# Performance work log

Measured on AMD Instinct MI355X. Metric: run time of the kernel, lower is better.

Reference implementation:

```python
import jax, jax.numpy as jnp
import numpy as np

D_MODEL, D_STATE, D_CONV, EXPAND, N_HEADS = 768, 64, 4, 2, 12
D_INNER = D_MODEL * EXPAND           # 1536
HEAD_DIM = D_INNER // N_HEADS        # 128
IN_PROJ = D_INNER * 2 + N_HEADS * D_STATE * 2 + N_HEADS  # 4620
EPS = 1e-5


def setup_inputs() -> dict:
    key = jax.random.key(0)
    ks = jax.random.split(key, 8)
    s = lambda fan_in: 1.0 / np.sqrt(fan_in)
    return {
        "x": jax.random.normal(ks[0], (1, 1024, D_MODEL), dtype=jnp.float32),
        "W_in": jax.random.normal(ks[1], (IN_PROJ, D_MODEL), dtype=jnp.float32) * s(D_MODEL),
        "conv_w": jax.random.normal(ks[2], (D_INNER, D_CONV), dtype=jnp.float32) * s(D_CONV),
        "conv_b": jnp.zeros((D_INNER,), dtype=jnp.float32),
        "A_log": jnp.full((N_HEADS,), np.log(0.5), dtype=jnp.float32),
        "Dp": jnp.ones((N_HEADS,), dtype=jnp.float32),
        "dt_bias": jnp.zeros((N_HEADS,), dtype=jnp.float32),
        "W_out": jax.random.normal(ks[3], (D_MODEL, D_INNER), dtype=jnp.float32) * s(D_INNER),
        "norm_w": jnp.ones((D_INNER,), dtype=jnp.float32),
    }


def _causal_conv1d(x, w, b):
    # x: (B,L,Din), depthwise causal conv with kernel size D_CONV
    L = x.shape[1]
    xp = jnp.pad(x, ((0, 0), (D_CONV - 1, 0), (0, 0)))
    y = b
    for i in range(D_CONV):  # fixed small kernel, unrolled
        y = y + xp[:, i:i + L, :] * w[:, i]
    return y


def reference(x, W_in, conv_w, conv_b, A_log, Dp, dt_bias, W_out, norm_w):
    B_sz, L, _ = x.shape
    nh, ds, hd = N_HEADS, D_STATE, HEAD_DIM
    proj = jnp.einsum('bld,pd->blp', x, W_in)
    z = proj[:, :, :D_INNER]
    x_ssm = proj[:, :, D_INNER:2 * D_INNER]
    o = 2 * D_INNER
    Bm = proj[:, :, o:o + nh * ds].reshape(B_sz, L, nh, ds)
    Cm = proj[:, :, o + nh * ds:o + 2 * nh * ds].reshape(B_sz, L, nh, ds)
    dt_r = proj[:, :, o + 2 * nh * ds:]
    dt = jax.nn.softplus(dt_r) + dt_bias[None, None, :]          # (B,L,nh)

    x_ssm = jax.nn.silu(_causal_conv1d(x_ssm, conv_w, conv_b))
    x_ssm = x_ssm.reshape(B_sz, L, nh, hd)

    A = -jnp.exp(A_log)                                          # (nh,)
    log_decay = A[None, None, :] * dt                            # (B,L,nh)
    Phi = jnp.cumsum(log_decay, axis=1)
    dB = dt[..., None] * Bm                                      # (B,L,nh,ds)
    # b: (B,L,nh,hd,ds) outer product
    b = dB[:, :, :, None, :] * x_ssm[..., None]
    max_exp = 80.0
    exp_neg_Phi = jnp.exp(jnp.minimum(-Phi, max_exp))[..., None, None]
    b_cumsum = jnp.cumsum(exp_neg_Phi * b, axis=1)
    h = jnp.exp(Phi)[..., None, None] * b_cumsum                 # (B,L,nh,hd,ds)
    y = jnp.sum(Cm[:, :, :, None, :] * h, axis=-1)               # (B,L,nh,hd)
    y = y + Dp[None, None, :, None] * x_ssm
    y = y.reshape(B_sz, L, D_INNER)

    # RMSNorm then gate
    rms = jax.lax.rsqrt(jnp.mean(y * y, axis=-1, keepdims=True) + EPS)
    y = y * rms * norm_w
    y = y * jax.nn.silu(z)
    return jnp.einsum('bli,di->bld', y, W_out)
```

## Files before the change

kernel.cpp:

```cpp
#include <hip/hip_runtime.h>
#include <cmath>

#define LSEQ   1024
#define NPROJ  4620
#define NPADW  4736
#define DINNER 1536
#define NH     12
#define HDIM   128
#define OFF_Z  0
#define OFF_X  1536
#define OFF_B  3072
#define OFF_C  3840
#define OFF_DT 4608

typedef unsigned short u16;
typedef unsigned int u32;
typedef short bf16x8 __attribute__((ext_vector_type(8)));
typedef float f32x4 __attribute__((ext_vector_type(4)));

__device__ inline u16 f2b(float f) {
  unsigned u = __float_as_uint(f);
  return (u16)((u + 0x7fffu + ((u >> 16) & 1u)) >> 16);
}
__device__ inline float b2f(u16 h) { return __uint_as_float(((unsigned)h) << 16); }
__device__ inline u32 pk2(float a, float b) { return (u32)f2b(a) | ((u32)f2b(b) << 16); }

__device__ inline void gll16(const void* g, void* l) {
  __builtin_amdgcn_global_load_lds((const __attribute__((address_space(1))) void*)g,
                                   (__attribute__((address_space(3))) void*)l, 16, 0, 0);
}

#define S0N 196608
#define S1N 909312
#define S1V 887040
#define S2N 294912
__global__ __launch_bounds__(256) void ksplit_all(const float* __restrict__ x,
    const float* __restrict__ Wi, const float* __restrict__ Wo,
    u16* __restrict__ Ah, u16* __restrict__ Wh, u16* __restrict__ Woh) {
  int i = blockIdx.x * 256 + threadIdx.x;
  const float* src; u16* hi; int j, valid;
  if (i < S0N)            { src = x;  hi = Ah;  j = i;              valid = S0N; }
  else if (i < S0N + S1N) { src = Wi; hi = Wh;  j = i - S0N;        valid = S1V; }
  else                    { src = Wo; hi = Woh; j = i - S0N - S1N;  valid = S2N; }
  float4 v = (j < valid) ? ((const float4*)src)[j] : make_float4(0.f, 0.f, 0.f, 0.f);
  ((uint2*)hi)[j] = make_uint2(pk2(v.x, v.y), pk2(v.z, v.w));
}

template<int BM, int BN, int MAP, bool NG>
__global__ __launch_bounds__(256) void gemm1(const u16* __restrict__ Ah,
    const u16* __restrict__ Wh, float* __restrict__ C,
    int lda, int ldw, int Ksl, int Nreal, int ldc) {
  constexpr int PLA = BM * 64;
  constexpr int IA = BM / 8, ITOT = IA + BN / 8;
  constexpr int FRn = BN / 32;
  __shared__ u16 lds[PLA + BN * 64];
  const int tid = threadIdx.x;
  const int l = tid & 63, w = tid >> 6;
  const int wm = w >> 1, wn = w & 1;
  const int kg = l >> 4, li = l & 15;

  int b = blockIdx.x, m0, n0, koff;
  float* Cp = C;
  if (MAP == 0) {
    int xcd = b & 7, idx = b >> 3;
    m0 = (idx & 15) * 64;
    n0 = (xcd * 5 + (idx >> 4)) * 128;
    koff = 0;
    if (NG && n0 >= NPADW) return;
  } else {
    int xcd = b & 7, idx = b >> 3;
    int gg = xcd * 6 + (idx >> 4);
    m0 = (idx & 15) * 64;
    n0 = (gg % 12) * 64;
    koff = (gg / 12) * 384;
    Cp = C + (size_t)(gg / 12) * LSEQ * ldc;
  }

  const int srcg = ((l & 7) ^ (l >> 3)) * 8;
  auto stage = [&](int t) {
    const int k0 = koff + t * 64;
    for (int q = w; q < ITOT; q += 4) {
      const u16* gb; int r0b, ldk, dst;
      if (q < IA) { gb = Ah; r0b = m0 + 8 * q;        dst = 8 * q * 64;              ldk = lda; }
      else        { gb = Wh; r0b = n0 + 8 * (q - IA); dst = PLA + 8 * (q - IA) * 64; ldk = ldw; }
      gll16(gb + (size_t)(r0b + (l >> 3)) * ldk + k0 + srcg, &lds[dst]);
    }
  };
  auto rd = [&](int region, int row, int ks) -> bf16x8 {
    return *(const bf16x8*)&lds[region + row * 64 + (((ks * 4 + kg) ^ (row & 7)) << 3)];
  };

  f32x4 acc[2][FRn];
#pragma unroll
  for (int m = 0; m < 2; ++m)
#pragma unroll
    for (int n = 0; n < FRn; ++n) acc[m][n] = (f32x4){0.f, 0.f, 0.f, 0.f};

  const int NT = Ksl / 64;
  stage(0);
  asm volatile("s_waitcnt vmcnt(0)" ::: "memory");
  __syncthreads();
  for (int t = 0; t < NT; ++t) {
    bf16x8 af[2][2], wf[FRn][2];
#pragma unroll
    for (int ks = 0; ks < 2; ++ks) {
#pragma unroll
      for (int m = 0; m < 2; ++m)
        af[m][ks] = rd(0, wm * 32 + m * 16 + li, ks);
#pragma unroll
      for (int n = 0; n < FRn; ++n)
        wf[n][ks] = rd(PLA, wn * (BN / 2) + n * 16 + li, ks);
    }
    __syncthreads();
    if (t + 1 < NT) stage(t + 1);
#pragma unroll
    for (int ks = 0; ks < 2; ++ks)
#pragma unroll
      for (int m = 0; m < 2; ++m)
#pragma unroll
        for (int n = 0; n < FRn; ++n)
          acc[m][n] = __builtin_amdgcn_mfma_f32_16x16x32_bf16(af[m][ks], wf[n][ks], acc[m][n], 0, 0, 0);
    if (t + 1 < NT) {
      asm volatile("s_waitcnt vmcnt(0)" ::: "memory");
      __syncthreads();
    }
  }
#pragma unroll
  for (int m = 0; m < 2; ++m) {
    int rbase = m0 + wm * 32 + m * 16 + kg * 4;
#pragma unroll
    for (int n = 0; n < FRn; ++n) {
      int col = n0 + wn * (BN / 2) + n * 16 + li;
      if (!NG || col < Nreal) {
#pragma unroll
        for (int r = 0; r < 4; ++r)
          Cp[(size_t)(rbase + r) * ldc + col] = acc[m][n][r];
      }
    }
  }
}

__global__ __launch_bounds__(256) void addk(const float* __restrict__ P,
    const float* __restrict__ rmsacc, float* __restrict__ out) {
  const int S = LSEQ * 768 / 4;
  int i = blockIdx.x * 256 + threadIdx.x;
  int t = i / 192;
  float rms = rsqrtf(rmsacc[t] * (1.f / 1536.f) + 1e-5f);
  float4 a = ((const float4*)P)[i];
  float4 b = ((const float4*)P)[i + S];
  float4 c = ((const float4*)P)[i + 2 * S];
  float4 d = ((const float4*)P)[i + 3 * S];
  ((float4*)out)[i] = make_float4((a.x + b.x + c.x + d.x) * rms,
                                  (a.y + b.y + c.y + d.y) * rms,
                                  (a.z + b.z + c.z + d.z) * rms,
                                  (a.w + b.w + c.w + d.w) * rms);
}

__global__ __launch_bounds__(256) void dtphi(const float* __restrict__ proj,
    const float* __restrict__ A_log, const float* __restrict__ dt_bias,
    float* __restrict__ Phi, float* __restrict__ dts, float* __restrict__ rmsacc) {
  int h = blockIdx.x, tid = threadIdx.x;
  if (h < 4) rmsacc[h * 256 + tid] = 0.f;
  float Ac = -expf(A_log[h]);
  float bb = dt_bias[h];
  float v[4], s = 0.f;
#pragma unroll
  for (int u = 0; u < 4; ++u) {
    int t = tid * 4 + u;
    float xr = proj[(size_t)t * NPROJ + OFF_DT + h];
    float sp = (xr > 20.f) ? xr : log1pf(expf(xr));
    v[u] = sp + bb;
    s += v[u];
  }
  int lane = tid & 63, wv = tid >> 6;
  float ps = s;
#pragma unroll
  for (int d = 1; d < 64; d <<= 1) {
    float o = __shfl_up(ps, d);
    if (lane >= d) ps += o;
  }
  __shared__ float wsum[4];
  if (lane == 63) wsum[wv] = ps;
  __syncthreads();
  float off = 0.f;
  for (int w = 0; w < wv; ++w) off += wsum[w];
  float run = off + ps - s;
#pragma unroll
  for (int u = 0; u < 4; ++u) {
    int t = tid * 4 + u;
    run += v[u];
    Phi[t * NH + h] = Ac * run;
    dts[t * NH + h] = v[u];
  }
}

__global__ __launch_bounds__(256) void conv_state(const float* __restrict__ proj,
    const float* __restrict__ cw, const float* __restrict__ cb,
    const float* __restrict__ Phi, const float* __restrict__ dts,
    u16* __restrict__ xactT, float* __restrict__ SlocF) {
  const int k = blockIdx.x, h = blockIdx.y, tid = threadIdx.x;
  const int l = tid & 63, w = tid >> 6, kg = l >> 4, li = l & 15;
  __shared__ u16 Bw[4096];
  __shared__ u16 Xt[8192];
  __shared__ float wS[64];
  const int s0 = k * 64;
  if (tid < 64) {
    float pe = Phi[(s0 + 63) * NH + h];
    float p  = Phi[(s0 + tid) * NH + h];
    wS[tid] = expf(pe + fminf(-p, 80.f)) * dts[(s0 + tid) * NH + h];
  }
  __syncthreads();
#pragma unroll
  for (int u = 0; u < 4; ++u) {
    int idx = tid + u * 256, s = idx >> 4, q = (idx & 15) * 4;
    float4 v = *(const float4*)(proj + (size_t)(s0 + s) * NPROJ + OFF_B + h * 64 + q);
    float ws_ = wS[s];
    float vv[4] = {v.x, v.y, v.z, v.w};
#pragma unroll
    for (int j = 0; j < 4; ++j) {
      int d = q + j;
      Bw[d * 64 + (((s >> 3) ^ (d & 7)) << 3) + (s & 7)] = f2b(vv[j] * ws_);
    }
  }
  {
    int c = tid & 127, th = tid >> 7;
    int cg = h * HDIM + c;
    float w0 = cw[cg * 4], w1 = cw[cg * 4 + 1], w2 = cw[cg * 4 + 2], w3 = cw[cg * 4 + 3];
    float bias = cb[cg];
    int tb = s0 + th * 32;
    auto P = [&](int t) { return (t >= 0) ? proj[(size_t)t * NPROJ + OFF_X + cg] : 0.f; };
    float x0 = P(tb - 3), x1 = P(tb - 2), x2 = P(tb - 1);
    u32 pkb[16];
    float prev = 0.f;
#pragma unroll
    for (int i = 0; i < 32; ++i) {
      float x3 = P(tb + i);
      float a = bias;
      a = fmaf(x0, w0, a); a = fmaf(x1, w1, a); a = fmaf(x2, w2, a); a = fmaf(x3, w3, a);
      float sv = a / (1.f + expf(-a));
      if (i & 1) pkb[i >> 1] = pk2(prev, sv); else prev = sv;
      x0 = x1; x1 = x2; x2 = x3;
    }
#pragma unroll
    for (int g = 0; g < 4; ++g) {
      int sg = th * 4 + g;
      *(uint4*)&Xt[c * 64 + ((sg ^ (c & 7)) << 3)] =
          make_uint4(pkb[g * 4], pkb[g * 4 + 1], pkb[g * 4 + 2], pkb[g * 4 + 3]);
    }
    size_t xo = ((size_t)(k * NH + h) * 128 + c) * 64 + th * 32;
#pragma unroll
    for (int g = 0; g < 4; ++g)
      *(uint4*)(xactT + xo + g * 8) =
          make_uint4(pkb[g * 4], pkb[g * 4 + 1], pkb[g * 4 + 2], pkb[g * 4 + 3]);
  }
  __syncthreads();
  const int wm = w >> 1, wn = w & 1;
  auto rd = [&](const u16* reg, int row, int ks) -> bf16x8 {
    return *(const bf16x8*)&reg[row * 64 + (((ks * 4 + kg) ^ (row & 7)) << 3)];
  };
  f32x4 acc[4][2];
#pragma unroll
  for (int m = 0; m < 4; ++m)
#pragma unroll
    for (int n = 0; n < 2; ++n) acc[m][n] = (f32x4){0.f, 0.f, 0.f, 0.f};
#pragma unroll
  for (int ks = 0; ks < 2; ++ks) {
    bf16x8 xf[4], bf[2];
#pragma unroll
    for (int m = 0; m < 4; ++m) xf[m] = rd(Xt, wm * 64 + m * 16 + li, ks);
#pragma unroll
    for (int n = 0; n < 2; ++n) bf[n] = rd(Bw, wn * 32 + n * 16 + li, ks);
#pragma unroll
    for (int m = 0; m < 4; ++m)
#pragma unroll
      for (int n = 0; n < 2; ++n)
        acc[m][n] = __builtin_amdgcn_mfma_f32_16x16x32_bf16(xf[m], bf[n], acc[m][n], 0, 0, 0);
  }
  float* dst = SlocF + (((size_t)(k * NH + h)) << 13);
#pragma unroll
  for (int m = 0; m < 4; ++m)
#pragma unroll
    for (int n = 0; n < 2; ++n)
#pragma unroll
      for (int r = 0; r < 4; ++r) {
        int c = wm * 64 + m * 16 + kg * 4 + r;
        int d = wn * 32 + n * 16 + li;
        dst[c * 64 + d] = acc[m][n][r];
      }
}

__global__ __launch_bounds__(256) void chunk_scan(const float* __restrict__ SlocF,
    u16* __restrict__ SlocT, const float* __restrict__ Phi) {
  int b = blockIdx.x;
  int h = b >> 5;
  int e = (b & 31) * 256 + threadIdx.x;
  float run = SlocF[((size_t)h << 13) + e];
  SlocT[((size_t)h << 13) + e] = f2b(run);
#pragma unroll
  for (int k = 1; k < 16; ++k) {
    float lam = expf(Phi[(k * 64 + 63) * NH + h] - Phi[(k * 64 - 1) * NH + h]);
    size_t o = ((size_t)(k * NH + h) << 13) + e;
    run = fmaf(lam, run, SlocF[o]);
    SlocT[o] = f2b(run);
  }
}

__global__ __launch_bounds__(256) void ssm_out(const float* __restrict__ proj,
    const u16* __restrict__ xactT, const float* __restrict__ Phi,
    const float* __restrict__ dts, const float* __restrict__ Dp,
    const u16* __restrict__ SlocT, const float* __restrict__ nw,
    u16* __restrict__ Yh, float* __restrict__ rmsacc) {
  const int k = blockIdx.x, h = blockIdx.y, zh = blockIdx.z, tid = threadIdx.x;
  const int l = tid & 63, w = tid >> 6, kg = l >> 4, li = l & 15;
  const int wm = w >> 1, wn = w & 1;
  __shared__ u16 Cs[4096], Bs[4096], Ps[4096], Xs[4096], Ss[4096];
  __shared__ float phiT[64], eSs[64], dSs[64], eTs[64];
  __shared__ float sq[64], nws[64];
  const int t0 = k * 64;
  const int srcg = ((l & 7) ^ (l >> 3)) * 8;
  {
#pragma unroll
    for (int j = 0; j < 2; ++j) {
      int rb = w * 16 + j * 8;
      gll16(xactT + ((size_t)(k * NH + h) * 128 + zh * 64 + rb + (l >> 3)) * 64 + srcg, &Xs[rb * 64]);
    }
    if (k > 0) {
      const u16* ssrc = SlocT + (((size_t)((k - 1) * NH + h) * 128 + zh * 64)) * 64;
#pragma unroll
      for (int j = 0; j < 2; ++j) {
        int rb = w * 16 + j * 8;
        gll16(ssrc + (size_t)(rb + (l >> 3)) * 64 + srcg, &Ss[rb * 64]);
      }
    }
  }
#pragma unroll
  for (int u = 0; u < 4; ++u) {
    int idx = tid + u * 256, i = idx >> 4, q = (idx & 15) * 4;
    int aoff = i * 64 + (((q >> 3) ^ (i & 7)) << 3) + (q & 4);
    float4 cv = *(const float4*)(proj + (size_t)(t0 + i) * NPROJ + OFF_C + h * 64 + q);
    float4 bv = *(const float4*)(proj + (size_t)(t0 + i) * NPROJ + OFF_B + h * 64 + q);
    *(uint2*)&Cs[aoff] = make_uint2(pk2(cv.x, cv.y), pk2(cv.z, cv.w));
    *(uint2*)&Bs[aoff] = make_uint2(pk2(bv.x, bv.y), pk2(bv.z, bv.w));
  }
  if (tid < 64) {
    float p = Phi[(t0 + tid) * NH + h];
    phiT[tid] = p;
    eSs[tid] = fminf(-p, 80.f);
    dSs[tid] = dts[(t0 + tid) * NH + h];
    eTs[tid] = (k > 0) ? expf(p - Phi[(t0 - 1) * NH + h]) : 0.f;
    sq[tid] = 0.f;
    nws[tid] = nw[h * HDIM + zh * 64 + tid];
  }
  __syncthreads();
  auto rd = [&](const u16* reg, int row, int ks) -> bf16x8 {
    return *(const bf16x8*)&reg[row * 64 + (((ks * 4 + kg) ^ (row & 7)) << 3)];
  };
  bf16x8 Cf[2][2];
  f32x4 accS[2][2];
#pragma unroll
  for (int m = 0; m < 2; ++m)
#pragma unroll
    for (int n = 0; n < 2; ++n) accS[m][n] = (f32x4){0.f, 0.f, 0.f, 0.f};
#pragma unroll
  for (int ks = 0; ks < 2; ++ks) {
    bf16x8 Bf[2];
#pragma unroll
    for (int m = 0; m < 2; ++m) Cf[m][ks] = rd(Cs, wm * 32 + m * 16 + li, ks);
#pragma unroll
    for (int n = 0; n < 2; ++n) Bf[n] = rd(Bs, wn * 32 + n * 16 + li, ks);
#pragma unroll
    for (int m = 0; m < 2; ++m)
#pragma unroll
      for (int n = 0; n < 2; ++n)
        accS[m][n] = __builtin_amdgcn_mfma_f32_16x16x32_bf16(Cf[m][ks], Bf[n], accS[m][n], 0, 0, 0);
  }
#pragma unroll
  for (int m = 0; m < 2; ++m)
#pragma unroll
    for (int n = 0; n < 2; ++n)
#pragma unroll
      for (int r = 0; r < 4; ++r) {
        int t = wm * 32 + m * 16 + kg * 4 + r;
        int s = wn * 32 + n * 16 + li;
        float f = (s <= t) ? expf(phiT[t] + eSs[s]) * dSs[s] : 0.f;
        Ps[t * 64 + (((s >> 3) ^ (t & 7)) << 3) + (s & 7)] = f2b(accS[m][n][r] * f);
      }
  __syncthreads();
  f32x4 accY[2][2], acc2[2][2];
#pragma unroll
  for (int m = 0; m < 2; ++m)
#pragma unroll
    for (int n = 0; n < 2; ++n) {
      accY[m][n] = (f32x4){0.f, 0.f, 0.f, 0.f};
      acc2[m][n] = (f32x4){0.f, 0.f, 0.f, 0.f};
    }
#pragma unroll
  for (int ks = 0; ks < 2; ++ks) {
    bf16x8 Pf[2], Xf[2];
#pragma unroll
    for (int m = 0; m < 2; ++m) Pf[m] = rd(Ps, wm * 32 + m * 16 + li, ks);
#pragma unroll
    for (int n = 0; n < 2; ++n) Xf[n] = rd(Xs, wn * 32 + n * 16 + li, ks);
#pragma unroll
    for (int m = 0; m < 2; ++m)
#pragma unroll
      for (int n = 0; n < 2; ++n)
        accY[m][n] = __builtin_amdgcn_mfma_f32_16x16x32_bf16(Pf[m], Xf[n], accY[m][n], 0, 0, 0);
    if (k > 0) {
      bf16x8 Sf[2];
#pragma unroll
      for (int n = 0; n < 2; ++n) Sf[n] = rd(Ss, wn * 32 + n * 16 + li, ks);
#pragma unroll
      for (int m = 0; m < 2; ++m)
#pragma unroll
        for (int n = 0; n < 2; ++n)
          acc2[m][n] = __builtin_amdgcn_mfma_f32_16x16x32_bf16(Cf[m][ks], Sf[n], acc2[m][n], 0, 0, 0);
    }
  }
  float dp = Dp[h];
  float ls[8] = {};
#pragma unroll
  for (int m = 0; m < 2; ++m)
#pragma unroll
    for (int n = 0; n < 2; ++n)
#pragma unroll
      for (int r = 0; r < 4; ++r) {
        int t = wm * 32 + m * 16 + kg * 4 + r;
        int c = wn * 32 + n * 16 + li;
        float xv = b2f(Xs[c * 64 + (((t >> 3) ^ (c & 7)) << 3) + (t & 7)]);
        float val = accY[m][n][r] + eTs[t] * acc2[m][n][r] + dp * xv;
        ls[m * 4 + r] = fmaf(val, val, ls[m * 4 + r]);
        float z = proj[(size_t)(t0 + t) * NPROJ + OFF_Z + h * HDIM + zh * 64 + c];
        float sz = z / (1.f + expf(-z));
        Yh[(size_t)(t0 + t) * DINNER + h * HDIM + zh * 64 + c] = f2b(val * nws[c] * sz);
      }
#pragma unroll
  for (int j = 0; j < 8; ++j) {
    float v = ls[j];
    v += __shfl_xor(v, 1); v += __shfl_xor(v, 2);
    v += __shfl_xor(v, 4); v += __shfl_xor(v, 8);
    if (li == 0) atomicAdd(&sq[wm * 32 + (j >> 2) * 16 + kg * 4 + (j & 3)], v);
  }
  __syncthreads();
  if (tid < 64) atomicAdd(&rmsacc[t0 + tid], sq[tid]);
}

extern "C" void kernel_launch(void* const* d_in, const int* in_sizes, int n_in,
                              void* d_out, int out_size, void* d_ws, size_t ws_size,
                              hipStream_t stream) {
  const float* x       = (const float*)d_in[0];
  const float* W_in    = (const float*)d_in[1];
  const float* conv_w  = (const float*)d_in[2];
  const float* conv_b  = (const float*)d_in[3];
  const float* A_log   = (const float*)d_in[4];
  const float* Dp      = (const float*)d_in[5];
  const float* dt_bias = (const float*)d_in[6];
  const float* W_out   = (const float*)d_in[7];
  const float* norm_w  = (const float*)d_in[8];
  float* out = (float*)d_out;

  char* base = (char*)d_ws;
  size_t o = 0;
  auto alloc = [&](size_t bytes) { char* r = base + o; o += (bytes + 255) & ~(size_t)255; return r; };
  float* proj   = (float*)alloc((size_t)LSEQ * NPROJ * 4);
  float* Phi    = (float*)alloc((size_t)LSEQ * NH * 4);
  float* dts    = (float*)alloc((size_t)LSEQ * NH * 4);
  float* rmsacc = (float*)alloc((size_t)LSEQ * 4);
  float* SlocF  = (float*)alloc((size_t)16 * NH * 8192 * 4);
  u16*   SlocT  = (u16*)alloc((size_t)16 * NH * 8192 * 2);
  u16*   xactT  = (u16*)alloc((size_t)16 * NH * 8192 * 2);
  u16*   Ah     = (u16*)alloc((size_t)LSEQ * 768 * 2);
  u16*   Wh     = (u16*)alloc((size_t)NPADW * 768 * 2);
  u16*   Woh    = (u16*)alloc((size_t)768 * DINNER * 2);
  u16*   Yh     = (u16*)alloc((size_t)LSEQ * DINNER * 2);
  float* Pp     = (float*)alloc((size_t)4 * LSEQ * 768 * 4);

  ksplit_all<<<dim3((S0N + S1N + S2N) / 256), 256, 0, stream>>>(
      x, W_in, W_out, Ah, Wh, Woh);
  gemm1<64, 128, 0, true><<<dim3(640), 256, 0, stream>>>(
      Ah, Wh, proj, 768, 768, 768, NPROJ, NPROJ);
  dtphi<<<dim3(NH), 256, 0, stream>>>(proj, A_log, dt_bias, Phi, dts, rmsacc);
  conv_state<<<dim3(16, NH), 256, 0, stream>>>(proj, conv_w, conv_b, Phi, dts, xactT, SlocF);
  chunk_scan<<<dim3(NH * 32), 256, 0, stream>>>(SlocF, SlocT, Phi);
  ssm_out<<<dim3(16, NH, 2), 256, 0, stream>>>(
      proj, xactT, Phi, dts, Dp, SlocT, norm_w, Yh, rmsacc);
  gemm1<64, 64, 1, false><<<dim3(768), 256, 0, stream>>>(
      Yh, Woh, Pp, 1536, 1536, 384, 768, 768);
  addk<<<dim3(LSEQ * 768 / 4 / 256), 256, 0, stream>>>(Pp, rmsacc, out);
}
```

Before: 69.34 us.

## Fuse dt/Phi scan into conv_state and move W_out conversion into chunk_scan

Removes the separate dtphi launch by having every conv_state block recompute the full per-head softplus and cumulative sum of dt. Each block keeps the 64 Phi/dt values for its own chunk in LDS and writes them out for later kernels. The W_out fp32-to-bf16 conversion moves from the up-front split kernel into chunk_scan, so it runs while chunk_scan does its memory-bound scan. This saves one kernel launch and shortens the critical path. In exchange the 1024-step dt scan is computed redundantly 16 times per head, and chunk_scan carries extra conversion traffic.

```diff
diff --git a/kernel.cpp b/kernel.cpp
--- a/kernel.cpp
+++ b/kernel.cpp
@@ -35,13 +35,11 @@
 #define S1V 887040
 #define S2N 294912
 __global__ __launch_bounds__(256) void ksplit_all(const float* __restrict__ x,
-    const float* __restrict__ Wi, const float* __restrict__ Wo,
-    u16* __restrict__ Ah, u16* __restrict__ Wh, u16* __restrict__ Woh) {
+    const float* __restrict__ Wi, u16* __restrict__ Ah, u16* __restrict__ Wh) {
   int i = blockIdx.x * 256 + threadIdx.x;
   const float* src; u16* hi; int j, valid;
-  if (i < S0N)            { src = x;  hi = Ah;  j = i;              valid = S0N; }
-  else if (i < S0N + S1N) { src = Wi; hi = Wh;  j = i - S0N;        valid = S1V; }
-  else                    { src = Wo; hi = Woh; j = i - S0N - S1N;  valid = S2N; }
+  if (i < S0N) { src = x;  hi = Ah; j = i;       valid = S0N; }
+  else         { src = Wi; hi = Wh; j = i - S0N; valid = S1V; }
   float4 v = (j < valid) ? ((const float4*)src)[j] : make_float4(0.f, 0.f, 0.f, 0.f);
   ((uint2*)hi)[j] = make_uint2(pk2(v.x, v.y), pk2(v.z, v.w));
 }
@@ -156,59 +154,60 @@
                                   (a.w + b.w + c.w + d.w) * rms);
 }
 
-__global__ __launch_bounds__(256) void dtphi(const float* __restrict__ proj,
-    const float* __restrict__ A_log, const float* __restrict__ dt_bias,
-    float* __restrict__ Phi, float* __restrict__ dts, float* __restrict__ rmsacc) {
-  int h = blockIdx.x, tid = threadIdx.x;
-  if (h < 4) rmsacc[h * 256 + tid] = 0.f;
-  float Ac = -expf(A_log[h]);
-  float bb = dt_bias[h];
-  float v[4], s = 0.f;
-#pragma unroll
-  for (int u = 0; u < 4; ++u) {
-    int t = tid * 4 + u;
-    float xr = proj[(size_t)t * NPROJ + OFF_DT + h];
-    float sp = (xr > 20.f) ? xr : log1pf(expf(xr));
-    v[u] = sp + bb;
-    s += v[u];
-  }
-  int lane = tid & 63, wv = tid >> 6;
-  float ps = s;
-#pragma unroll
-  for (int d = 1; d < 64; d <<= 1) {
-    float o = __shfl_up(ps, d);
-    if (lane >= d) ps += o;
-  }
-  __shared__ float wsum[4];
-  if (lane == 63) wsum[wv] = ps;
-  __syncthreads();
-  float off = 0.f;
-  for (int w = 0; w < wv; ++w) off += wsum[w];
-  float run = off + ps - s;
-#pragma unroll
-  for (int u = 0; u < 4; ++u) {
-    int t = tid * 4 + u;
-    run += v[u];
-    Phi[t * NH + h] = Ac * run;
-    dts[t * NH + h] = v[u];
-  }
-}
-
 __global__ __launch_bounds__(256) void conv_state(const float* __restrict__ proj,
     const float* __restrict__ cw, const float* __restrict__ cb,
-    const float* __restrict__ Phi, const float* __restrict__ dts,
-    u16* __restrict__ xactT, float* __restrict__ SlocF) {
+    const float* __restrict__ A_log, const float* __restrict__ dt_bias,
+    u16* __restrict__ xactT, float* __restrict__ SlocF,
+    float* __restrict__ Phi, float* __restrict__ dts, float* __restrict__ rmsacc) {
   const int k = blockIdx.x, h = blockIdx.y, tid = threadIdx.x;
   const int l = tid & 63, w = tid >> 6, kg = l >> 4, li = l & 15;
   __shared__ u16 Bw[4096];
   __shared__ u16 Xt[8192];
   __shared__ float wS[64];
+  __shared__ float wsum[4];
+  __shared__ float phiC[64], dtC[64];
   const int s0 = k * 64;
-  if (tid < 64) {
-    float pe = Phi[(s0 + 63) * NH + h];
-    float p  = Phi[(s0 + tid) * NH + h];
-    wS[tid] = expf(pe + fminf(-p, 80.f)) * dts[(s0 + tid) * NH + h];
-  }
+
+  if (h == 0 && tid < 64) rmsacc[k * 64 + tid] = 0.f;
+  {
+    float Ac = -expf(A_log[h]);
+    float bb = dt_bias[h];
+    float v[4], s = 0.f;
+#pragma unroll
+    for (int u = 0; u < 4; ++u) {
+      int t = tid * 4 + u;
+      float xr = proj[(size_t)t * NPROJ + OFF_DT + h];
+      float sp = (xr > 20.f) ? xr : log1pf(expf(xr));
+      v[u] = sp + bb;
+      s += v[u];
+    }
+    int lane = tid & 63, wv = tid >> 6;
+    float ps = s;
+#pragma unroll
+    for (int d = 1; d < 64; d <<= 1) {
+      float o = __shfl_up(ps, d);
+      if (lane >= d) ps += o;
+    }
+    if (lane == 63) wsum[wv] = ps;
+    __syncthreads();
+    float off = 0.f;
+    for (int q = 0; q < wv; ++q) off += wsum[q];
+    float run = off + ps - s;
+#pragma unroll
+    for (int u = 0; u < 4; ++u) {
+      int t = tid * 4 + u;
+      run += v[u];
+      if ((t >> 6) == k) {
+        float ph = Ac * run;
+        phiC[t & 63] = ph;
+        dtC[t & 63] = v[u];
+        Phi[t * NH + h] = ph;
+        dts[t * NH + h] = v[u];
+      }
+    }
+  }
+  __syncthreads();
+  if (tid < 64) wS[tid] = expf(phiC[63] + fminf(-phiC[tid], 80.f)) * dtC[tid];
   __syncthreads();
 #pragma unroll
   for (int u = 0; u < 4; ++u) {
@@ -290,7 +289,15 @@
 }
 
 __global__ __launch_bounds__(256) void chunk_scan(const float* __restrict__ SlocF,
-    u16* __restrict__ SlocT, const float* __restrict__ Phi) {
+    u16* __restrict__ SlocT, const float* __restrict__ Phi,
+    const float* __restrict__ Wo, u16* __restrict__ Woh) {
+  int gi = blockIdx.x * 256 + threadIdx.x;
+#pragma unroll
+  for (int it = 0; it < 3; ++it) {
+    int j = gi + it * 98304;
+    float4 vv = ((const float4*)Wo)[j];
+    ((uint2*)Woh)[j] = make_uint2(pk2(vv.x, vv.y), pk2(vv.z, vv.w));
+  }
   int b = blockIdx.x;
   int h = b >> 5;
   int e = (b & 31) * 256 + threadIdx.x;
@@ -475,13 +482,12 @@
   u16*   Yh     = (u16*)alloc((size_t)LSEQ * DINNER * 2);
   float* Pp     = (float*)alloc((size_t)4 * LSEQ * 768 * 4);
 
-  ksplit_all<<<dim3((S0N + S1N + S2N) / 256), 256, 0, stream>>>(
-      x, W_in, W_out, Ah, Wh, Woh);
+  ksplit_all<<<dim3((S0N + S1N) / 256), 256, 0, stream>>>(x, W_in, Ah, Wh);
   gemm1<64, 128, 0, true><<<dim3(640), 256, 0, stream>>>(
       Ah, Wh, proj, 768, 768, 768, NPROJ, NPROJ);
-  dtphi<<<dim3(NH), 256, 0, stream>>>(proj, A_log, dt_bias, Phi, dts, rmsacc);
-  conv_state<<<dim3(16, NH), 256, 0, stream>>>(proj, conv_w, conv_b, Phi, dts, xactT, SlocF);
-  chunk_scan<<<dim3(NH * 32), 256, 0, stream>>>(SlocF, SlocT, Phi);
+  conv_state<<<dim3(16, NH), 256, 0, stream>>>(
+      proj, conv_w, conv_b, A_log, dt_bias, xactT, SlocF, Phi, dts, rmsacc);
+  chunk_scan<<<dim3(NH * 32), 256, 0, stream>>>(SlocF, SlocT, Phi, W_out, Woh);
   ssm_out<<<dim3(16, NH, 2), 256, 0, stream>>>(
       proj, xactT, Phi, dts, Dp, SlocT, norm_w, Yh, rmsacc);
   gemm1<64, 64, 1, false><<<dim3(768), 256, 0, stream>>>(
```

Result: faster. 66.83 us (-3.6%).
